# Optimization experiments

Measured on AMD Instinct MI355X. Metric: run time of the kernel, lower is better.

## Reference

```python
import jax, jax.numpy as jnp
import numpy as np

REG_MAX = 16
NUM_CLASSES = 80
STRIDES = (8, 16, 32)
FEAT_SIZES = ((80, 80), (40, 40), (20, 20))
CLS_DIM = 256
REG_DIM = 256
B = 16


def setup_inputs() -> dict:
    key = jax.random.key(0)
    ks = jax.random.split(key, 32)
    inp = {}
    i = 0
    for l, (H, W) in enumerate(FEAT_SIZES):
        inp[f"cls_feat{l}"] = jax.random.normal(ks[i], (B, CLS_DIM, H, W), jnp.float32); i += 1
        inp[f"reg_feat{l}"] = jax.random.normal(ks[i], (B, REG_DIM, H, W), jnp.float32); i += 1
    bias_init = -float(np.log((1.0 - 0.01) / 0.01))
    for l in range(3):
        inp[f"obj_w{l}"] = jax.random.normal(ks[i], (1, REG_DIM), jnp.float32) * 0.02; i += 1
        inp[f"obj_b{l}"] = jnp.full((1,), bias_init, jnp.float32)
        inp[f"cls_w{l}"] = jax.random.normal(ks[i], (NUM_CLASSES, CLS_DIM), jnp.float32) * 0.02; i += 1
        inp[f"cls_b{l}"] = jnp.full((NUM_CLASSES,), bias_init, jnp.float32)
        inp[f"reg_w{l}"] = jax.random.normal(ks[i], (4 * REG_MAX, REG_DIM), jnp.float32) * 0.02; i += 1
        inp[f"reg_b{l}"] = jnp.ones((4 * REG_MAX,), jnp.float32)
    return inp


def _anchors(H, W, stride):
    ay, ax = jnp.meshgrid(jnp.arange(H, dtype=jnp.float32), jnp.arange(W, dtype=jnp.float32), indexing="ij")
    a = jnp.stack([ax, ay], axis=-1).reshape(-1, 2)  # [HW, 2] (x, y)
    return (a + 0.5) * stride


def _level(cls_feat, reg_feat, obj_w, obj_b, cls_w, cls_b, reg_w, reg_b, stride):
    Bb, _, H, W = cls_feat.shape
    M = H * W
    # 1x1 convs as channel contractions; output in [B, H, W, O] then flatten to [B, M, O]
    obj = (jnp.einsum("bchw,oc->bhwo", reg_feat, obj_w) + obj_b).reshape(Bb, M, 1)
    cls = (jnp.einsum("bchw,oc->bhwo", cls_feat, cls_w) + cls_b).reshape(Bb, M, NUM_CLASSES)
    reg = (jnp.einsum("bchw,oc->bhwo", reg_feat, reg_w) + reg_b).reshape(Bb, M, 4 * REG_MAX)
    # DFL decode: softmax over bins, expectation with proj = linspace(0, reg_max, reg_max)
    proj = jnp.linspace(0.0, float(REG_MAX), REG_MAX)
    dist = jax.nn.softmax(reg.reshape(Bb, M, 4, REG_MAX), axis=-1)
    reg_d = jnp.einsum("bmfr,r->bmf", dist, proj)  # [B, M, 4] (l, t, r, b)
    anchors = _anchors(H, W, stride)  # [M, 2]
    x1y1 = anchors[None] - reg_d[..., :2] * stride
    x2y2 = anchors[None] + reg_d[..., 2:] * stride
    box = jnp.concatenate([x1y1, x2y2], axis=-1)  # [B, M, 4]
    return jnp.concatenate([obj, cls, reg, box], axis=-1)  # [B, M, 1+80+64+4]


def reference(cls_feat0, cls_feat1, cls_feat2, reg_feat0, reg_feat1, reg_feat2,
              obj_w0, obj_b0, cls_w0, cls_b0, reg_w0, reg_b0,
              obj_w1, obj_b1, cls_w1, cls_b1, reg_w1, reg_b1,
              obj_w2, obj_b2, cls_w2, cls_b2, reg_w2, reg_b2):
    lvl0 = _level(cls_feat0, reg_feat0, obj_w0, obj_b0, cls_w0, cls_b0, reg_w0, reg_b0, STRIDES[0])
    lvl1 = _level(cls_feat1, reg_feat1, obj_w1, obj_b1, cls_w1, cls_b1, reg_w1, reg_b1, STRIDES[1])
    lvl2 = _level(cls_feat2, reg_feat2, obj_w2, obj_b2, cls_w2, cls_b2, reg_w2, reg_b2, STRIDES[2])
    # concat anchors along M: [B, 8400, 149]
    return jnp.concatenate([lvl0, lvl1, lvl2], axis=1)
```

## Files before the change

kernel.cpp:

```cpp
#include <hip/hip_runtime.h>
#include <stdint.h>

typedef __attribute__((ext_vector_type(4))) float f32x4;
typedef __attribute__((ext_vector_type(8))) short s16x8;

struct Params {
  const float* cls_feat[3];
  const float* reg_feat[3];
  const float* obj_w[3];
  const float* obj_b[3];
  const float* cls_w[3];
  const float* cls_b[3];
  const float* reg_w[3];
  const float* reg_b[3];
  float* out;
};

__device__ __forceinline__ unsigned short f2bf(float f) {
  unsigned int u = __builtin_bit_cast(unsigned int, f);
  u = (u + 0x7FFFu + ((u >> 16) & 1u)) >> 16;
  return (unsigned short)u;
}

#define LDS_PITCH 264

__global__ __launch_bounds__(320) void head_kernel(Params p) {
  const int tid  = threadIdx.x;
  const int lane = tid & 63;
  const int wave = tid >> 6;
  const int quad = lane >> 4;
  const int col  = lane & 15;
  const bool is_cls = (blockIdx.y == 0);

  int bx = blockIdx.x;
  int b  = bx / 132;
  int t  = bx - b * 132;
  int level, tloc;
  if (t < 100)      { level = 0; tloc = t; }
  else if (t < 125) { level = 1; tloc = t - 100; }
  else              { level = 2; tloc = t - 125; }

  const int   LW_[3]   = {80, 40, 20};
  const int   LM_[3]   = {6400, 1600, 400};
  const float LS_[3]   = {8.f, 16.f, 32.f};
  const int   LOFF_[3] = {0, 6400, 8000};

  const int   Mlvl = LM_[level];
  const int   Moff = LOFF_[level];
  const float strd = LS_[level];
  const int   m0   = tloc * 64;
  int valid = Mlvl - m0; if (valid > 64) valid = 64;

  __shared__ __align__(16) short lds_feat[64 * LDS_PITCH];
  __shared__ float g_lds[4][64];

  const float* featp = (is_cls ? p.cls_feat[level] : p.reg_feat[level])
                       + (size_t)b * 256 * (size_t)Mlvl;
  {
    const int mloc = tid & 63;
    int mg = m0 + mloc; if (mg > Mlvl - 1) mg = Mlvl - 1;
    const float* colp = featp + mg;
    for (int cb = wave; cb < 32; cb += 5) {
      const int c0 = cb * 8;
      float f[8];
      #pragma unroll
      for (int j = 0; j < 8; ++j) f[j] = colp[(size_t)(c0 + j) * Mlvl];
      s16x8 h;
      #pragma unroll
      for (int j = 0; j < 8; ++j) h[j] = (short)f2bf(f[j]);
      *(s16x8*)&lds_feat[mloc * LDS_PITCH + c0] = h;
    }
  }

  s16x8 afrag[8];
  {
    const int orow = wave * 16 + col;
    const float* wptr = nullptr;
    if (is_cls) {
      wptr = p.cls_w[level] + orow * 256;
    } else {
      if (orow < 64)       wptr = p.reg_w[level] + orow * 256;
      else if (orow == 64) wptr = p.obj_w[level];
    }
    #pragma unroll
    for (int s = 0; s < 8; ++s) {
      s16x8 a = {0, 0, 0, 0, 0, 0, 0, 0};
      if (wptr) {
        const f32x4* wp = (const f32x4*)(wptr + s * 32 + quad * 8);
        f32x4 w0 = wp[0], w1 = wp[1];
        a[0] = (short)f2bf(w0[0]); a[1] = (short)f2bf(w0[1]);
        a[2] = (short)f2bf(w0[2]); a[3] = (short)f2bf(w0[3]);
        a[4] = (short)f2bf(w1[0]); a[5] = (short)f2bf(w1[1]);
        a[6] = (short)f2bf(w1[2]); a[7] = (short)f2bf(w1[3]);
      }
      afrag[s] = a;
    }
  }

  float bias[4];
  #pragma unroll
  for (int r = 0; r < 4; ++r) {
    const int o = wave * 16 + quad * 4 + r;
    if (is_cls) bias[r] = p.cls_b[level][o];
    else        bias[r] = (o < 64) ? p.reg_b[level][o]
                        : ((o == 64) ? p.obj_b[level][0] : 0.f);
  }

  __syncthreads();

  f32x4 acc[4];
  #pragma unroll
  for (int mf = 0; mf < 4; ++mf) {
    f32x4 d = {0.f, 0.f, 0.f, 0.f};
    const short* brow = &lds_feat[(mf * 16 + col) * LDS_PITCH + quad * 8];
    #pragma unroll
    for (int s = 0; s < 8; ++s) {
      s16x8 bfrag = *(const s16x8*)(brow + s * 32);
      d = __builtin_amdgcn_mfma_f32_16x16x32_bf16(afrag[s], bfrag, d, 0, 0, 0);
    }
    acc[mf] = d;
  }

  const size_t outbase = (size_t)b * 8400 + Moff + m0;
  float* out = p.out;

  if (is_cls) {
    #pragma unroll
    for (int mf = 0; mf < 4; ++mf) {
      const int m = mf * 16 + col;
      if (m < valid) {
        const size_t rowp = (outbase + m) * 149 + 1 + wave * 16 + quad * 4;
        #pragma unroll
        for (int r = 0; r < 4; ++r) out[rowp + r] = acc[mf][r] + bias[r];
      }
    }
  } else if (wave < 4) {
    const float projscale = 16.f / 15.f;
    #pragma unroll
    for (int mf = 0; mf < 4; ++mf) {
      const int m = mf * 16 + col;
      const float v0 = acc[mf][0] + bias[0];
      const float v1 = acc[mf][1] + bias[1];
      const float v2 = acc[mf][2] + bias[2];
      const float v3 = acc[mf][3] + bias[3];
      if (m < valid) {
        const size_t rowp = (outbase + m) * 149 + 81 + wave * 16 + quad * 4;
        out[rowp + 0] = v0; out[rowp + 1] = v1;
        out[rowp + 2] = v2; out[rowp + 3] = v3;
      }
      float mx = fmaxf(fmaxf(v0, v1), fmaxf(v2, v3));
      mx = fmaxf(mx, __shfl_xor(mx, 16, 64));
      mx = fmaxf(mx, __shfl_xor(mx, 32, 64));
      const float e0 = __expf(v0 - mx), e1 = __expf(v1 - mx);
      const float e2 = __expf(v2 - mx), e3 = __expf(v3 - mx);
      float s = e0 + e1 + e2 + e3;
      const float q4 = (float)(quad * 4);
      float n = q4 * e0 + (q4 + 1.f) * e1 + (q4 + 2.f) * e2 + (q4 + 3.f) * e3;
      s += __shfl_xor(s, 16, 64); s += __shfl_xor(s, 32, 64);
      n += __shfl_xor(n, 16, 64); n += __shfl_xor(n, 32, 64);
      if (quad == 0) g_lds[wave][m] = projscale * n / s;
    }
  } else {
    #pragma unroll
    for (int mf = 0; mf < 4; ++mf) {
      const int m = mf * 16 + col;
      if (quad == 0 && m < valid)
        out[(outbase + m) * 149] = acc[mf][0] + bias[0];
    }
  }

  __syncthreads();

  if (!is_cls && wave == 4) {
    const int m = lane;
    if (m < valid) {
      const float g0 = g_lds[0][m], g1 = g_lds[1][m];
      const float g2 = g_lds[2][m], g3 = g_lds[3][m];
      const int mg = m0 + m;
      int hh;
      if (level == 0)      hh = mg / 80;
      else if (level == 1) hh = mg / 40;
      else                 hh = mg / 20;
      const int ww = mg - hh * LW_[level];
      const float ax = (ww + 0.5f) * strd;
      const float ay = (hh + 0.5f) * strd;
      const size_t rowp = (outbase + m) * 149 + 145;
      out[rowp + 0] = ax - g0 * strd;
      out[rowp + 1] = ay - g1 * strd;
      out[rowp + 2] = ax + g2 * strd;
      out[rowp + 3] = ay + g3 * strd;
    }
  }
}

extern "C" void kernel_launch(void* const* d_in, const int* in_sizes, int n_in,
                              void* d_out, int out_size, void* d_ws, size_t ws_size,
                              hipStream_t stream) {
  (void)in_sizes; (void)n_in; (void)out_size; (void)d_ws; (void)ws_size;
  Params p;
  p.cls_feat[0] = (const float*)d_in[0];
  p.reg_feat[0] = (const float*)d_in[1];
  p.cls_feat[1] = (const float*)d_in[2];
  p.reg_feat[1] = (const float*)d_in[3];
  p.cls_feat[2] = (const float*)d_in[4];
  p.reg_feat[2] = (const float*)d_in[5];
  for (int l = 0; l < 3; ++l) {
    const int base = 6 + l * 6;
    p.obj_w[l] = (const float*)d_in[base + 0];
    p.obj_b[l] = (const float*)d_in[base + 1];
    p.cls_w[l] = (const float*)d_in[base + 2];
    p.cls_b[l] = (const float*)d_in[base + 3];
    p.reg_w[l] = (const float*)d_in[base + 4];
    p.reg_b[l] = (const float*)d_in[base + 5];
  }
  p.out = (float*)d_out;

  dim3 grid(16 * 132, 2);
  dim3 block(320);
  hipLaunchKernelGGL(head_kernel, grid, block, 0, stream, p);
}
```

Before: 377.2 us.

## Precompute bf16 weights and give each wave an independent 16-anchor tile

```diff
diff --git a/kernel.cpp b/kernel.cpp
--- a/kernel.cpp
+++ b/kernel.cpp
@@ -3,6 +3,8 @@
 
 typedef __attribute__((ext_vector_type(4))) float f32x4;
 typedef __attribute__((ext_vector_type(8))) short s16x8;
+typedef float f32x4u __attribute__((ext_vector_type(4), aligned(4)));
+typedef unsigned short u16x4 __attribute__((ext_vector_type(4)));
 
 struct Params {
   const float* cls_feat[3];
@@ -13,6 +15,7 @@
   const float* cls_b[3];
   const float* reg_w[3];
   const float* reg_b[3];
+  unsigned short* wbf;
   float* out;
 };
 
@@ -22,181 +25,123 @@
   return (unsigned short)u;
 }
 
-#define LDS_PITCH 264
+__global__ __launch_bounds__(64) void prep_weights(Params p) {
+  const int R = blockIdx.x;
+  const int kind  = R / 240;
+  const int rem   = R - kind * 240;
+  const int level = rem / 80;
+  const int o     = rem - level * 80;
+  const float* src = nullptr;
+  if (kind == 0)      src = p.cls_w[level] + (size_t)o * 256;
+  else if (o < 64)    src = p.reg_w[level] + (size_t)o * 256;
+  else if (o == 64)   src = p.obj_w[level];
+  unsigned short* dst = p.wbf + (size_t)R * 256 + threadIdx.x * 4;
+  u16x4 h = {0, 0, 0, 0};
+  if (src) {
+    f32x4 f = *(const f32x4u*)(src + threadIdx.x * 4);
+    h[0] = f2bf(f[0]); h[1] = f2bf(f[1]); h[2] = f2bf(f[2]); h[3] = f2bf(f[3]);
+  }
+  *(u16x4*)dst = h;
+}
 
-__global__ __launch_bounds__(320) void head_kernel(Params p) {
+__global__ __launch_bounds__(256) void head_kernel(Params p) {
   const int tid  = threadIdx.x;
   const int lane = tid & 63;
   const int wave = tid >> 6;
   const int quad = lane >> 4;
   const int col  = lane & 15;
-  const bool is_cls = (blockIdx.y == 0);
+  const int kind = blockIdx.y;
 
-  int bx = blockIdx.x;
-  int b  = bx / 132;
-  int t  = bx - b * 132;
-  int level, tloc;
-  if (t < 100)      { level = 0; tloc = t; }
-  else if (t < 125) { level = 1; tloc = t - 100; }
-  else              { level = 2; tloc = t - 125; }
+  const int t = blockIdx.x * 4 + wave;
+  const int b = t / 525;
+  const int r = t - b * 525;
+  int level, m0;
+  if (r < 400)      { level = 0; m0 = r * 16; }
+  else if (r < 500) { level = 1; m0 = (r - 400) * 16; }
+  else              { level = 2; m0 = (r - 500) * 16; }
 
+  const int   LM_[3]   = {6400, 1600, 400};
   const int   LW_[3]   = {80, 40, 20};
-  const int   LM_[3]   = {6400, 1600, 400};
   const float LS_[3]   = {8.f, 16.f, 32.f};
   const int   LOFF_[3] = {0, 6400, 8000};
+  const int   Mlvl = LM_[level];
+  const float strd = LS_[level];
 
-  const int   Mlvl = LM_[level];
-  const int   Moff = LOFF_[level];
-  const float strd = LS_[level];
-  const int   m0   = tloc * 64;
-  int valid = Mlvl - m0; if (valid > 64) valid = 64;
-
-  __shared__ __align__(16) short lds_feat[64 * LDS_PITCH];
-  __shared__ float g_lds[4][64];
-
-  const float* featp = (is_cls ? p.cls_feat[level] : p.reg_feat[level])
-                       + (size_t)b * 256 * (size_t)Mlvl;
-  {
-    const int mloc = tid & 63;
-    int mg = m0 + mloc; if (mg > Mlvl - 1) mg = Mlvl - 1;
-    const float* colp = featp + mg;
-    for (int cb = wave; cb < 32; cb += 5) {
-      const int c0 = cb * 8;
-      float f[8];
-      #pragma unroll
-      for (int j = 0; j < 8; ++j) f[j] = colp[(size_t)(c0 + j) * Mlvl];
-      s16x8 h;
-      #pragma unroll
-      for (int j = 0; j < 8; ++j) h[j] = (short)f2bf(f[j]);
-      *(s16x8*)&lds_feat[mloc * LDS_PITCH + c0] = h;
-    }
+  const float* feat = (kind ? p.reg_feat[level] : p.cls_feat[level])
+                      + (size_t)b * 256 * (size_t)Mlvl + m0 + col;
+  s16x8 bfrag[8];
+  #pragma unroll
+  for (int s = 0; s < 8; ++s) {
+    float f[8];
+    #pragma unroll
+    for (int j = 0; j < 8; ++j)
+      f[j] = feat[(size_t)(s * 32 + quad * 8 + j) * Mlvl];
+    s16x8 h;
+    #pragma unroll
+    for (int j = 0; j < 8; ++j) h[j] = (short)f2bf(f[j]);
+    bfrag[s] = h;
   }
 
-  s16x8 afrag[8];
-  {
-    const int orow = wave * 16 + col;
-    const float* wptr = nullptr;
-    if (is_cls) {
-      wptr = p.cls_w[level] + orow * 256;
-    } else {
-      if (orow < 64)       wptr = p.reg_w[level] + orow * 256;
-      else if (orow == 64) wptr = p.obj_w[level];
-    }
+  const unsigned short* wbase = p.wbf + (size_t)((kind * 3 + level) * 80) * 256;
+  const size_t outbase = (size_t)b * 8400 + LOFF_[level] + m0;
+  float* out = p.out;
+  const size_t rowoff = (outbase + col) * 149;
+
+  float g[4];
+
+  #pragma unroll
+  for (int tile = 0; tile < 5; ++tile) {
+    const unsigned short* wp = wbase + (size_t)(tile * 16 + col) * 256 + quad * 8;
+    f32x4 d = {0.f, 0.f, 0.f, 0.f};
     #pragma unroll
     for (int s = 0; s < 8; ++s) {
-      s16x8 a = {0, 0, 0, 0, 0, 0, 0, 0};
-      if (wptr) {
-        const f32x4* wp = (const f32x4*)(wptr + s * 32 + quad * 8);
-        f32x4 w0 = wp[0], w1 = wp[1];
-        a[0] = (short)f2bf(w0[0]); a[1] = (short)f2bf(w0[1]);
-        a[2] = (short)f2bf(w0[2]); a[3] = (short)f2bf(w0[3]);
-        a[4] = (short)f2bf(w1[0]); a[5] = (short)f2bf(w1[1]);
-        a[6] = (short)f2bf(w1[2]); a[7] = (short)f2bf(w1[3]);
-      }
-      afrag[s] = a;
+      s16x8 a = *(const s16x8*)(wp + s * 32);
+      d = __builtin_amdgcn_mfma_f32_16x16x32_bf16(a, bfrag[s], d, 0, 0, 0);
     }
-  }
 
-  float bias[4];
-  #pragma unroll
-  for (int r = 0; r < 4; ++r) {
-    const int o = wave * 16 + quad * 4 + r;
-    if (is_cls) bias[r] = p.cls_b[level][o];
-    else        bias[r] = (o < 64) ? p.reg_b[level][o]
-                        : ((o == 64) ? p.obj_b[level][0] : 0.f);
-  }
-
-  __syncthreads();
-
-  f32x4 acc[4];
-  #pragma unroll
-  for (int mf = 0; mf < 4; ++mf) {
-    f32x4 d = {0.f, 0.f, 0.f, 0.f};
-    const short* brow = &lds_feat[(mf * 16 + col) * LDS_PITCH + quad * 8];
-    #pragma unroll
-    for (int s = 0; s < 8; ++s) {
-      s16x8 bfrag = *(const s16x8*)(brow + s * 32);
-      d = __builtin_amdgcn_mfma_f32_16x16x32_bf16(afrag[s], bfrag, d, 0, 0, 0);
-    }
-    acc[mf] = d;
-  }
-
-  const size_t outbase = (size_t)b * 8400 + Moff + m0;
-  float* out = p.out;
-
-  if (is_cls) {
-    #pragma unroll
-    for (int mf = 0; mf < 4; ++mf) {
-      const int m = mf * 16 + col;
-      if (m < valid) {
-        const size_t rowp = (outbase + m) * 149 + 1 + wave * 16 + quad * 4;
-        #pragma unroll
-        for (int r = 0; r < 4; ++r) out[rowp + r] = acc[mf][r] + bias[r];
-      }
-    }
-  } else if (wave < 4) {
-    const float projscale = 16.f / 15.f;
-    #pragma unroll
-    for (int mf = 0; mf < 4; ++mf) {
-      const int m = mf * 16 + col;
-      const float v0 = acc[mf][0] + bias[0];
-      const float v1 = acc[mf][1] + bias[1];
-      const float v2 = acc[mf][2] + bias[2];
-      const float v3 = acc[mf][3] + bias[3];
-      if (m < valid) {
-        const size_t rowp = (outbase + m) * 149 + 81 + wave * 16 + quad * 4;
-        out[rowp + 0] = v0; out[rowp + 1] = v1;
-        out[rowp + 2] = v2; out[rowp + 3] = v3;
-      }
-      float mx = fmaxf(fmaxf(v0, v1), fmaxf(v2, v3));
+    if (kind == 0) {
+      f32x4 bias = *(const f32x4u*)(p.cls_b[level] + tile * 16 + quad * 4);
+      f32x4 v = d + bias;
+      *(f32x4u*)(out + rowoff + 1 + tile * 16 + quad * 4) = v;
+    } else if (tile < 4) {
+      f32x4 bias = *(const f32x4u*)(p.reg_b[level] + tile * 16 + quad * 4);
+      f32x4 v = d + bias;
+      *(f32x4u*)(out + rowoff + 81 + tile * 16 + quad * 4) = v;
+      float mx = fmaxf(fmaxf(v[0], v[1]), fmaxf(v[2], v[3]));
       mx = fmaxf(mx, __shfl_xor(mx, 16, 64));
       mx = fmaxf(mx, __shfl_xor(mx, 32, 64));
-      const float e0 = __expf(v0 - mx), e1 = __expf(v1 - mx);
-      const float e2 = __expf(v2 - mx), e3 = __expf(v3 - mx);
+      const float e0 = __expf(v[0] - mx), e1 = __expf(v[1] - mx);
+      const float e2 = __expf(v[2] - mx), e3 = __expf(v[3] - mx);
       float s = e0 + e1 + e2 + e3;
       const float q4 = (float)(quad * 4);
       float n = q4 * e0 + (q4 + 1.f) * e1 + (q4 + 2.f) * e2 + (q4 + 3.f) * e3;
       s += __shfl_xor(s, 16, 64); s += __shfl_xor(s, 32, 64);
       n += __shfl_xor(n, 16, 64); n += __shfl_xor(n, 32, 64);
-      if (quad == 0) g_lds[wave][m] = projscale * n / s;
-    }
-  } else {
-    #pragma unroll
-    for (int mf = 0; mf < 4; ++mf) {
-      const int m = mf * 16 + col;
-      if (quad == 0 && m < valid)
-        out[(outbase + m) * 149] = acc[mf][0] + bias[0];
+      g[tile] = (16.f / 15.f) * n / s;
+    } else {
+      if (quad == 0) out[rowoff] = d[0] + p.obj_b[level][0];
     }
   }
 
-  __syncthreads();
-
-  if (!is_cls && wave == 4) {
-    const int m = lane;
-    if (m < valid) {
-      const float g0 = g_lds[0][m], g1 = g_lds[1][m];
-      const float g2 = g_lds[2][m], g3 = g_lds[3][m];
-      const int mg = m0 + m;
-      int hh;
-      if (level == 0)      hh = mg / 80;
-      else if (level == 1) hh = mg / 40;
-      else                 hh = mg / 20;
-      const int ww = mg - hh * LW_[level];
-      const float ax = (ww + 0.5f) * strd;
-      const float ay = (hh + 0.5f) * strd;
-      const size_t rowp = (outbase + m) * 149 + 145;
-      out[rowp + 0] = ax - g0 * strd;
-      out[rowp + 1] = ay - g1 * strd;
-      out[rowp + 2] = ax + g2 * strd;
-      out[rowp + 3] = ay + g3 * strd;
-    }
+  if (kind == 1 && quad == 1) {
+    const int mg = m0 + col;
+    const int hh = mg / LW_[level];
+    const int ww = mg - hh * LW_[level];
+    const float ax = (ww + 0.5f) * strd;
+    const float ay = (hh + 0.5f) * strd;
+    f32x4 box;
+    box[0] = ax - g[0] * strd;
+    box[1] = ay - g[1] * strd;
+    box[2] = ax + g[2] * strd;
+    box[3] = ay + g[3] * strd;
+    *(f32x4u*)(out + rowoff + 145) = box;
   }
 }
 
 extern "C" void kernel_launch(void* const* d_in, const int* in_sizes, int n_in,
                               void* d_out, int out_size, void* d_ws, size_t ws_size,
                               hipStream_t stream) {
-  (void)in_sizes; (void)n_in; (void)out_size; (void)d_ws; (void)ws_size;
+  (void)in_sizes; (void)n_in; (void)out_size; (void)ws_size;
   Params p;
   p.cls_feat[0] = (const float*)d_in[0];
   p.reg_feat[0] = (const float*)d_in[1];
@@ -213,9 +158,9 @@
     p.reg_w[l] = (const float*)d_in[base + 4];
     p.reg_b[l] = (const float*)d_in[base + 5];
   }
+  p.wbf = (unsigned short*)d_ws;
   p.out = (float*)d_out;
 
-  dim3 grid(16 * 132, 2);
-  dim3 block(320);
-  hipLaunchKernelGGL(head_kernel, grid, block, 0, stream, p);
+  hipLaunchKernelGGL(prep_weights, dim3(480), dim3(64), 0, stream, p);
+  hipLaunchKernelGGL(head_kernel, dim3(2100, 2), dim3(256), 0, stream, p);
 }
```

New measurement: 397.8 us. 5.5% more time.
